# Kernel tuning notes

Hardware: AMD Instinct MI355X
Metric: run time of the kernel (lower is better)

The kernel has to match this reference:

```python
import jax, jax.numpy as jnp
import numpy as np

B, N_ATOMS, N_BONDS, HID = 16, 50000, 100000, 128


def _lin(x, w, b):
    # torch nn.Linear: y = x @ W^T + b
    return x @ w.T + b


def setup_inputs() -> dict:
    key = jax.random.key(0)
    ks = jax.random.split(key, 16)

    def w(k, shape, fan_in):
        return jax.random.normal(k, shape, jnp.float32) * (1.0 / np.sqrt(fan_in))

    return {
        "alpha": jax.random.normal(ks[0], (B, 1), jnp.float32),
        "baseline_positions": jax.random.normal(ks[1], (B, N_ATOMS, 3), jnp.float32),
        "bonds": jax.random.randint(ks[2], (N_BONDS, 2), 0, N_ATOMS, jnp.int32),
        # standard branch: Linear(1,256) -> ResBlock(256) x2 -> Linear(256, n_atoms*3)
        "w_in": w(ks[3], (256, 1), 1), "b_in": jnp.zeros((256,), jnp.float32),
        "rb1_w1": w(ks[4], (256, 256), 256), "rb1_b1": jnp.zeros((256,), jnp.float32),
        "rb1_w2": w(ks[5], (256, 256), 256), "rb1_b2": jnp.zeros((256,), jnp.float32),
        "rb2_w1": w(ks[6], (256, 256), 256), "rb2_b1": jnp.zeros((256,), jnp.float32),
        "rb2_w2": w(ks[7], (256, 256), 256), "rb2_b2": jnp.zeros((256,), jnp.float32),
        "w_out": w(ks[8], (N_ATOMS * 3, 256), 256), "b_out": jnp.zeros((N_ATOMS * 3,), jnp.float32),
        # graph branch
        "msg_w": w(ks[9], (HID, 3), 3), "msg_b": jnp.zeros((HID,), jnp.float32),
        "upd_w": w(ks[10], (3, HID), HID), "upd_b": jnp.zeros((3,), jnp.float32),
        "go_w": w(ks[11], (3, 3), 3), "go_b": jnp.zeros((3,), jnp.float32),
    }


def reference(alpha, baseline_positions, bonds,
              w_in, b_in,
              rb1_w1, rb1_b1, rb1_w2, rb1_b2,
              rb2_w1, rb2_b1, rb2_w2, rb2_b2,
              w_out, b_out,
              msg_w, msg_b, upd_w, upd_b, go_w, go_b):
    b, n_atoms, _ = baseline_positions.shape

    # ---- standard branch (Dropout is identity in eval mode) ----
    x = jax.nn.relu(_lin(alpha, w_in, b_in))
    x = jax.nn.relu(_lin(jax.nn.relu(_lin(x, rb1_w1, rb1_b1)), rb1_w2, rb1_b2) + x)
    x = jax.nn.relu(_lin(jax.nn.relu(_lin(x, rb2_w1, rb2_b1)), rb2_w2, rb2_b2) + x)
    standard_out = _lin(x, w_out, b_out).reshape(b, n_atoms, 3)

    # ---- graph branch: symmetric edge list, mean aggregation ----
    src = jnp.concatenate([bonds[:, 0], bonds[:, 1]])  # [2E]
    dst = jnp.concatenate([bonds[:, 1], bonds[:, 0]])  # [2E]
    deg = jnp.zeros((n_atoms,), jnp.float32).at[dst].add(1.0)
    safe_deg = jnp.maximum(deg, 1.0)[None, :, None]
    has_nb = (deg > 0)[None, :, None]

    h = baseline_positions
    for _ in range(2):  # n_iters
        # mean of linear(neighbor feats) == linear(mean of neighbor feats) (affine)
        nb_sum = jnp.zeros((b, n_atoms, 3), h.dtype).at[:, dst, :].add(h[:, src, :])
        nb_mean = nb_sum / safe_deg
        msgs = jnp.where(has_nb, _lin(nb_mean, msg_w, msg_b), 0.0)  # [B,N,128]
        h = h + _lin(msgs, upd_w, upd_b)

    graph_out = _lin(h, go_w, go_b)
    return standard_out + graph_out
```

## Files before the change

kernel.cpp:

```cpp
#include <hip/hip_runtime.h>

#define N_ATOMS 50000
#define N_BONDS 100000
#define BATCH   16
#define N3      150000
#define BK      32

#define X_OFF    0
#define MC_OFF   4096
#define CNT_OFF  4112
#define BKT_OFF  54112
#define HA_OFF   1654112
#define HB_OFF   4054112
#define WS_FAST_BYTES ((size_t)(HB_OFF + 2400000) * 4)

#define DEGF_OFF 4112
#define HT_OFF   54144
#define NB_OFF   2454144


__device__ __forceinline__ void mlp_block(int b, int j,
    const float* __restrict__ alpha,
    const float* __restrict__ w_in, const float* __restrict__ b_in,
    const float* __restrict__ w1a, const float* __restrict__ b1a,
    const float* __restrict__ w1b, const float* __restrict__ b1b,
    const float* __restrict__ w2a, const float* __restrict__ b2a,
    const float* __restrict__ w2b, const float* __restrict__ b2b,
    float* xs, float* ts, float* __restrict__ x_out)
{
    float v = fmaxf(w_in[j] * alpha[b] + b_in[j], 0.f);
    xs[j] = v;
    __syncthreads();

    float acc = b1a[j];
    const float4* wr = reinterpret_cast<const float4*>(w1a + j * 256);
    #pragma unroll 8
    for (int k4 = 0; k4 < 64; ++k4) {
        float4 w = wr[k4];
        acc += w.x * xs[4*k4] + w.y * xs[4*k4+1] + w.z * xs[4*k4+2] + w.w * xs[4*k4+3];
    }
    ts[j] = fmaxf(acc, 0.f);
    __syncthreads();

    acc = b1b[j] + xs[j];
    wr = reinterpret_cast<const float4*>(w1b + j * 256);
    #pragma unroll 8
    for (int k4 = 0; k4 < 64; ++k4) {
        float4 w = wr[k4];
        acc += w.x * ts[4*k4] + w.y * ts[4*k4+1] + w.z * ts[4*k4+2] + w.w * ts[4*k4+3];
    }
    v = fmaxf(acc, 0.f);
    __syncthreads();
    xs[j] = v;
    __syncthreads();

    acc = b2a[j];
    wr = reinterpret_cast<const float4*>(w2a + j * 256);
    #pragma unroll 8
    for (int k4 = 0; k4 < 64; ++k4) {
        float4 w = wr[k4];
        acc += w.x * xs[4*k4] + w.y * xs[4*k4+1] + w.z * xs[4*k4+2] + w.w * xs[4*k4+3];
    }
    ts[j] = fmaxf(acc, 0.f);
    __syncthreads();

    acc = b2b[j] + xs[j];
    wr = reinterpret_cast<const float4*>(w2b + j * 256);
    #pragma unroll 8
    for (int k4 = 0; k4 < 64; ++k4) {
        float4 w = wr[k4];
        acc += w.x * ts[4*k4] + w.y * ts[4*k4+1] + w.z * ts[4*k4+2] + w.w * ts[4*k4+3];
    }
    x_out[b * 256 + j] = fmaxf(acc, 0.f);
}

struct PrepParams {
    const float *alpha, *pos;
    const float *w_in, *b_in, *w1a, *b1a, *w1b, *b1b, *w2a, *b2a, *w2b, *b2b;
    const float *msg_w, *msg_b, *upd_w, *upd_b;
    float *x, *mc;
    int *cnt;
    float *hA;
};

__global__ __launch_bounds__(256) void prep_kernel(PrepParams p)
{
    __shared__ float smem[512];
    const int bid = blockIdx.x, tid = threadIdx.x;
    const int nb = gridDim.x;

    if (bid < 16) {
        mlp_block(bid, tid, p.alpha, p.w_in, p.b_in,
                  p.w1a, p.b1a, p.w1b, p.b1b, p.w2a, p.b2a, p.w2b, p.b2b,
                  smem, smem + 256, p.x);
    } else if (bid == 16) {
        if (tid < 9) {
            int d = tid / 3, dp = tid % 3;
            float s = 0.f;
            for (int k = 0; k < 128; ++k) s += p.upd_w[d*128 + k] * p.msg_w[k*3 + dp];
            p.mc[tid] = s;
        } else if (tid < 12) {
            int d = tid - 9;
            float s = p.upd_b[d];
            for (int k = 0; k < 128; ++k) s += p.upd_w[d*128 + k] * p.msg_b[k];
            p.mc[9 + d] = s;
        }
    } else {
        const int i0 = (bid - 17) * 256 + tid;
        const int st = (nb - 17) * 256;
        if (i0 < N_ATOMS / 4)
            ((int4*)p.cnt)[i0] = make_int4(0, 0, 0, 0);
        for (int i = i0; i < N_ATOMS * 48; i += st) {
            int n = i / 48, c = i - n * 48;
            int b = c / 3, d = c - b * 3;
            p.hA[i] = p.pos[(b * N_ATOMS + n) * 3 + d];
        }
    }
}

__global__ void fill_kernel(const int* __restrict__ bonds, int* __restrict__ cnt,
                            int* __restrict__ bucket)
{
    int e = blockIdx.x * blockDim.x + threadIdx.x;
    if (e >= N_BONDS) return;
    int a = bonds[2*e], b = bonds[2*e + 1];
    int sa = atomicAdd(cnt + a, 1);
    if (sa < BK) bucket[a * BK + sa] = b;
    int sb = atomicAdd(cnt + b, 1);
    if (sb < BK) bucket[b * BK + sb] = a;
}

__global__ void gather_kernel(const int* __restrict__ cnt, const int* __restrict__ bucket,
                              const float* __restrict__ mc, const float* __restrict__ upd_b,
                              const float* __restrict__ h_in, float* __restrict__ h_out)
{
    int t = blockIdx.x * blockDim.x + threadIdx.x;
    if (t >= N_ATOMS * BATCH) return;
    int n = t >> 4, b = t & 15;
    int dg = cnt[n];
    int base = n * 48 + b * 3;
    float d0, d1, d2;
    if (dg > 0) {
        int m = dg > BK ? BK : dg;
        float s0 = 0.f, s1 = 0.f, s2 = 0.f;
        const int* bk = bucket + n * BK;
        for (int j = 0; j < m; ++j) {
            const float* hs = h_in + bk[j] * 48 + b * 3;
            s0 += hs[0]; s1 += hs[1]; s2 += hs[2];
        }
        float inv = 1.f / (float)dg;
        s0 *= inv; s1 *= inv; s2 *= inv;
        d0 = mc[9]  + mc[0]*s0 + mc[1]*s1 + mc[2]*s2;
        d1 = mc[10] + mc[3]*s0 + mc[4]*s1 + mc[5]*s2;
        d2 = mc[11] + mc[6]*s0 + mc[7]*s1 + mc[8]*s2;
    } else {
        d0 = upd_b[0]; d1 = upd_b[1]; d2 = upd_b[2];
    }
    h_out[base]     = h_in[base]     + d0;
    h_out[base + 1] = h_in[base + 1] + d1;
    h_out[base + 2] = h_in[base + 2] + d2;
}

__global__ __launch_bounds__(128) void out_kernel(
    const float* __restrict__ w_out, const float* __restrict__ b_out,
    const float* __restrict__ x, const float* __restrict__ h_t,
    const float* __restrict__ go_w, const float* __restrict__ go_b,
    float* __restrict__ out)
{
    __shared__ float4 xs[1024];
    const int tid = threadIdx.x;
    const float4* xv = reinterpret_cast<const float4*>(x);
    #pragma unroll
    for (int i = 0; i < 8; ++i) xs[tid + i * 128] = xv[tid + i * 128];
    __syncthreads();

    const int r = blockIdx.x * 128 + tid;
    if (r >= N3) return;

    const float4* wr = reinterpret_cast<const float4*>(w_out + (size_t)r * 256);

    float acc[16];
    #pragma unroll
    for (int b = 0; b < 16; ++b) acc[b] = 0.f;

    float4 wbuf[16];
    #pragma unroll
    for (int i = 0; i < 16; ++i) wbuf[i] = wr[i];

    #pragma unroll 1
    for (int c = 0; c < 4; ++c) {
        float4 wcur[16];
        #pragma unroll
        for (int i = 0; i < 16; ++i) wcur[i] = wbuf[i];
        if (c < 3) {
            #pragma unroll
            for (int i = 0; i < 16; ++i) wbuf[i] = wr[(c + 1) * 16 + i];
        }
        #pragma unroll
        for (int i = 0; i < 16; ++i) {
            const int k4 = c * 16 + i;
            #pragma unroll
            for (int b = 0; b < 16; ++b) {
                float4 xf = xs[b * 64 + k4];
                acc[b] += wcur[i].x * xf.x + wcur[i].y * xf.y
                        + wcur[i].z * xf.z + wcur[i].w * xf.w;
            }
        }
    }

    const int n = r / 3, d = r - 3 * n;
    const float g0 = go_w[d*3], g1 = go_w[d*3 + 1], g2 = go_w[d*3 + 2];
    const float gb = go_b[d] + b_out[r];
    const float* hb = h_t + n * 48;
    #pragma unroll
    for (int b = 0; b < 16; ++b) {
        float g = gb + g0 * hb[b*3] + g1 * hb[b*3 + 1] + g2 * hb[b*3 + 2];
        out[(size_t)b * N3 + r] = acc[b] + g;
    }
}

__global__ void zero4_kernel(int4* __restrict__ p, int n4)
{
    int t = blockIdx.x * 256 + threadIdx.x;
    if (t < n4) p[t] = make_int4(0, 0, 0, 0);
}

__global__ void mlp_head_kernel(const float* __restrict__ alpha,
    const float* __restrict__ w_in, const float* __restrict__ b_in,
    const float* __restrict__ w1a, const float* __restrict__ b1a,
    const float* __restrict__ w1b, const float* __restrict__ b1b,
    const float* __restrict__ w2a, const float* __restrict__ b2a,
    const float* __restrict__ w2b, const float* __restrict__ b2b,
    const float* __restrict__ msg_w, const float* __restrict__ msg_b,
    const float* __restrict__ upd_w, const float* __restrict__ upd_b,
    float* __restrict__ x_out, float* __restrict__ mc)
{
    const int b = blockIdx.x, j = threadIdx.x;
    if (b == 16) {
        if (j < 9) {
            int d = j / 3, dp = j % 3;
            float s = 0.f;
            for (int k = 0; k < 128; ++k) s += upd_w[d*128 + k] * msg_w[k*3 + dp];
            mc[j] = s;
        } else if (j < 12) {
            int d = j - 9;
            float s = upd_b[d];
            for (int k = 0; k < 128; ++k) s += upd_w[d*128 + k] * msg_b[k];
            mc[9 + d] = s;
        }
        return;
    }
    __shared__ float xs[256];
    __shared__ float ts[256];
    mlp_block(b, j, alpha, w_in, b_in, w1a, b1a, w1b, b1b, w2a, b2a, w2b, b2b,
              xs, ts, x_out);
}

__global__ void transpose_in_kernel(const float* __restrict__ pos, float* __restrict__ h_t)
{
    int t = blockIdx.x * blockDim.x + threadIdx.x;
    if (t >= N_ATOMS * 48) return;
    int n = t / 48, c = t % 48;
    int b = c / 3, d = c % 3;
    h_t[t] = pos[(b * N_ATOMS + n) * 3 + d];
}

__global__ void degf_kernel(const int* __restrict__ bonds, float* __restrict__ deg)
{
    int e = blockIdx.x * blockDim.x + threadIdx.x;
    if (e >= N_BONDS) return;
    atomicAdd(deg + bonds[2*e],     1.f);
    atomicAdd(deg + bonds[2*e + 1], 1.f);
}

__global__ void scatter_kernel(const int* __restrict__ bonds,
                               const float* __restrict__ h_t, float* __restrict__ nb_t)
{
    int t = blockIdx.x * 192 + threadIdx.x;
    int e = t / 48, c = t % 48;
    if (e >= N_BONDS) return;
    int a  = bonds[2*e];
    int bb = bonds[2*e + 1];
    float va = h_t[a  * 48 + c];
    float vb = h_t[bb * 48 + c];
    atomicAdd(nb_t + bb * 48 + c, va);
    atomicAdd(nb_t + a  * 48 + c, vb);
}

__global__ void update_kernel(const float* __restrict__ nb_t, const float* __restrict__ deg,
                              const float* __restrict__ mc, const float* __restrict__ upd_b,
                              float* __restrict__ h_t)
{
    int t = blockIdx.x * blockDim.x + threadIdx.x;
    if (t >= N_ATOMS * BATCH) return;
    int n = t >> 4;
    int base = n * 48 + (t & 15) * 3;
    float dg = deg[n];
    float d0, d1, d2;
    if (dg > 0.f) {
        float inv = 1.f / dg;
        float m0 = nb_t[base] * inv, m1 = nb_t[base+1] * inv, m2 = nb_t[base+2] * inv;
        d0 = mc[9]  + mc[0]*m0 + mc[1]*m1 + mc[2]*m2;
        d1 = mc[10] + mc[3]*m0 + mc[4]*m1 + mc[5]*m2;
        d2 = mc[11] + mc[6]*m0 + mc[7]*m1 + mc[8]*m2;
    } else {
        d0 = upd_b[0]; d1 = upd_b[1]; d2 = upd_b[2];
    }
    h_t[base]     += d0;
    h_t[base + 1] += d1;
    h_t[base + 2] += d2;
}

extern "C" void kernel_launch(void* const* d_in, const int* in_sizes, int n_in,
                              void* d_out, int out_size, void* d_ws, size_t ws_size,
                              hipStream_t stream)
{
    const float* alpha = (const float*)d_in[0];
    const float* pos   = (const float*)d_in[1];
    const int*   bonds = (const int*)  d_in[2];
    const float* w_in  = (const float*)d_in[3];
    const float* b_in  = (const float*)d_in[4];
    const float* w1a   = (const float*)d_in[5];
    const float* b1a   = (const float*)d_in[6];
    const float* w1b   = (const float*)d_in[7];
    const float* b1b   = (const float*)d_in[8];
    const float* w2a   = (const float*)d_in[9];
    const float* b2a   = (const float*)d_in[10];
    const float* w2b   = (const float*)d_in[11];
    const float* b2b   = (const float*)d_in[12];
    const float* w_out = (const float*)d_in[13];
    const float* b_out = (const float*)d_in[14];
    const float* msg_w = (const float*)d_in[15];
    const float* msg_b = (const float*)d_in[16];
    const float* upd_w = (const float*)d_in[17];
    const float* upd_b = (const float*)d_in[18];
    const float* go_w  = (const float*)d_in[19];
    const float* go_b  = (const float*)d_in[20];

    float* out = (float*)d_out;
    float* ws  = (float*)d_ws;
    float* x   = ws + X_OFF;
    float* mc  = ws + MC_OFF;

    float* h_final;
    if (ws_size >= WS_FAST_BYTES) {
        PrepParams pp;
        pp.alpha = alpha; pp.pos = pos;
        pp.w_in = w_in; pp.b_in = b_in;
        pp.w1a = w1a; pp.b1a = b1a; pp.w1b = w1b; pp.b1b = b1b;
        pp.w2a = w2a; pp.b2a = b2a; pp.w2b = w2b; pp.b2b = b2b;
        pp.msg_w = msg_w; pp.msg_b = msg_b; pp.upd_w = upd_w; pp.upd_b = upd_b;
        pp.x = x; pp.mc = mc;
        pp.cnt = (int*)(ws + CNT_OFF);
        pp.hA  = ws + HA_OFF;
        prep_kernel<<<1024, 256, 0, stream>>>(pp);

        int* cnt    = (int*)(ws + CNT_OFF);
        int* bucket = (int*)(ws + BKT_OFF);
        float* hA   = ws + HA_OFF;
        float* hB   = ws + HB_OFF;

        fill_kernel<<<(N_BONDS + 255) / 256, 256, 0, stream>>>(bonds, cnt, bucket);
        gather_kernel<<<(N_ATOMS * BATCH + 255) / 256, 256, 0, stream>>>(cnt, bucket, mc, upd_b, hA, hB);
        gather_kernel<<<(N_ATOMS * BATCH + 255) / 256, 256, 0, stream>>>(cnt, bucket, mc, upd_b, hB, hA);
        h_final = hA;
    } else {
        float* degf = ws + DEGF_OFF;
        float* h_t  = ws + HT_OFF;
        size_t need_full = (size_t)(NB_OFF + N_ATOMS * 48) * sizeof(float);
        float* nb_t = (ws_size >= need_full) ? (ws + NB_OFF) : out;

        mlp_head_kernel<<<17, 256, 0, stream>>>(alpha, w_in, b_in,
                                                w1a, b1a, w1b, b1b,
                                                w2a, b2a, w2b, b2b,
                                                msg_w, msg_b, upd_w, upd_b, x, mc);
        zero4_kernel<<<(N_ATOMS / 4 + 255) / 256, 256, 0, stream>>>((int4*)degf, N_ATOMS / 4);
        degf_kernel<<<(N_BONDS + 255) / 256, 256, 0, stream>>>(bonds, degf);
        transpose_in_kernel<<<(N_ATOMS * 48 + 255) / 256, 256, 0, stream>>>(pos, h_t);
        for (int it = 0; it < 2; ++it) {
            zero4_kernel<<<(N_ATOMS * 48 / 4 + 255) / 256, 256, 0, stream>>>((int4*)nb_t, N_ATOMS * 48 / 4);
            scatter_kernel<<<25000, 192, 0, stream>>>(bonds, h_t, nb_t);
            update_kernel<<<(N_ATOMS * BATCH + 255) / 256, 256, 0, stream>>>(nb_t, degf, mc, upd_b, h_t);
        }
        h_final = h_t;
    }

    out_kernel<<<(N3 + 127) / 128, 128, 0, stream>>>(w_out, b_out, x, h_final, go_w, go_b, out);
}
```

Before: 133.1 us.

## Use bf16 MFMA for output projection GEMM

Rewrites the final output-projection kernel so each wave runs 16x16x32 bf16 MFMA instructions over the 16-batch by 150000-row product. Activations and weights are converted from fp32 to bf16 in registers, and the shared-memory staging of the activations is removed. Each wave now handles four 16-row tiles, with launch geometry changed to match. The aim is to replace scalar FMA work with matrix-core throughput; the cost is lower precision on a 256-deep reduction, and the per-lane row-strided weight loads may coalesce less well.

```diff
diff --git a/kernel.cpp b/kernel.cpp
--- a/kernel.cpp
+++ b/kernel.cpp
@@ -17,6 +17,9 @@
 #define DEGF_OFF 4112
 #define HT_OFF   54144
 #define NB_OFF   2454144
+
+typedef __bf16 bf16x8 __attribute__((ext_vector_type(8)));
+typedef float  f32x4  __attribute__((ext_vector_type(4)));
 
 
 __device__ __forceinline__ void mlp_block(int b, int j,
@@ -161,61 +164,58 @@
     h_out[base + 2] = h_in[base + 2] + d2;
 }
 
-__global__ __launch_bounds__(128) void out_kernel(
+__global__ __launch_bounds__(256) void out_kernel(
     const float* __restrict__ w_out, const float* __restrict__ b_out,
     const float* __restrict__ x, const float* __restrict__ h_t,
     const float* __restrict__ go_w, const float* __restrict__ go_b,
     float* __restrict__ out)
 {
-    __shared__ float4 xs[1024];
-    const int tid = threadIdx.x;
-    const float4* xv = reinterpret_cast<const float4*>(x);
+    const int lane = threadIdx.x & 63;
+    const int widx = threadIdx.x >> 6;
+    const int wave = blockIdx.x * 4 + widx;
+    const int g  = lane >> 4;
+    const int mn = lane & 15;
+
+    bf16x8 afrag[8];
+    const float* xrow = x + mn * 256 + g * 8;
     #pragma unroll
-    for (int i = 0; i < 8; ++i) xs[tid + i * 128] = xv[tid + i * 128];
-    __syncthreads();
-
-    const int r = blockIdx.x * 128 + tid;
-    if (r >= N3) return;
-
-    const float4* wr = reinterpret_cast<const float4*>(w_out + (size_t)r * 256);
-
-    float acc[16];
-    #pragma unroll
-    for (int b = 0; b < 16; ++b) acc[b] = 0.f;
-
-    float4 wbuf[16];
-    #pragma unroll
-    for (int i = 0; i < 16; ++i) wbuf[i] = wr[i];
+    for (int kb = 0; kb < 8; ++kb) {
+        float4 lo = *reinterpret_cast<const float4*>(xrow + kb * 32);
+        float4 hi = *reinterpret_cast<const float4*>(xrow + kb * 32 + 4);
+        bf16x8 a;
+        a[0] = (__bf16)lo.x; a[1] = (__bf16)lo.y; a[2] = (__bf16)lo.z; a[3] = (__bf16)lo.w;
+        a[4] = (__bf16)hi.x; a[5] = (__bf16)hi.y; a[6] = (__bf16)hi.z; a[7] = (__bf16)hi.w;
+        afrag[kb] = a;
+    }
 
     #pragma unroll 1
-    for (int c = 0; c < 4; ++c) {
-        float4 wcur[16];
+    for (int t = 0; t < 4; ++t) {
+        const int tile = wave * 4 + t;
+        if (tile >= 9375) break;
+        const int r = tile * 16 + mn;
+        const float* wrow = w_out + (size_t)r * 256 + g * 8;
+
+        f32x4 acc = {0.f, 0.f, 0.f, 0.f};
         #pragma unroll
-        for (int i = 0; i < 16; ++i) wcur[i] = wbuf[i];
-        if (c < 3) {
-            #pragma unroll
-            for (int i = 0; i < 16; ++i) wbuf[i] = wr[(c + 1) * 16 + i];
-        }
+        for (int kb = 0; kb < 8; ++kb) {
+            float4 lo = *reinterpret_cast<const float4*>(wrow + kb * 32);
+            float4 hi = *reinterpret_cast<const float4*>(wrow + kb * 32 + 4);
+            bf16x8 bfr;
+            bfr[0] = (__bf16)lo.x; bfr[1] = (__bf16)lo.y; bfr[2] = (__bf16)lo.z; bfr[3] = (__bf16)lo.w;
+            bfr[4] = (__bf16)hi.x; bfr[5] = (__bf16)hi.y; bfr[6] = (__bf16)hi.z; bfr[7] = (__bf16)hi.w;
+            acc = __builtin_amdgcn_mfma_f32_16x16x32_bf16(afrag[kb], bfr, acc, 0, 0, 0);
+        }
+
+        const int n = r / 3, d = r - 3 * n;
+        const float g0 = go_w[d*3], g1 = go_w[d*3 + 1], g2 = go_w[d*3 + 2];
+        const float gb = go_b[d] + b_out[r];
         #pragma unroll
-        for (int i = 0; i < 16; ++i) {
-            const int k4 = c * 16 + i;
-            #pragma unroll
-            for (int b = 0; b < 16; ++b) {
-                float4 xf = xs[b * 64 + k4];
-                acc[b] += wcur[i].x * xf.x + wcur[i].y * xf.y
-                        + wcur[i].z * xf.z + wcur[i].w * xf.w;
-            }
-        }
-    }
-
-    const int n = r / 3, d = r - 3 * n;
-    const float g0 = go_w[d*3], g1 = go_w[d*3 + 1], g2 = go_w[d*3 + 2];
-    const float gb = go_b[d] + b_out[r];
-    const float* hb = h_t + n * 48;
-    #pragma unroll
-    for (int b = 0; b < 16; ++b) {
-        float g = gb + g0 * hb[b*3] + g1 * hb[b*3 + 1] + g2 * hb[b*3 + 2];
-        out[(size_t)b * N3 + r] = acc[b] + g;
+        for (int j = 0; j < 4; ++j) {
+            const int b = g * 4 + j;
+            const float* hb = h_t + n * 48 + b * 3;
+            float gaff = gb + g0 * hb[0] + g1 * hb[1] + g2 * hb[2];
+            out[(size_t)b * N3 + r] = acc[j] + gaff;
+        }
     }
 }
 
@@ -385,5 +385,5 @@
         h_final = h_t;
     }
 
-    out_kernel<<<(N3 + 127) / 128, 128, 0, stream>>>(w_out, b_out, x, h_final, go_w, go_b, out);
-}
+    out_kernel<<<586, 256, 0, stream>>>(w_out, b_out, x, h_final, go_w, go_b, out);
+}
```

Measured after the change: 116.6 us. 12.4% less time.
